# Performance work log

Measured on AMD Instinct MI355X. Metric: run time of the kernel, lower is better.

Reference implementation:

```python
import jax, jax.numpy as jnp
import numpy as np

H = 32          # num_attention_heads
KVH = 8         # num_key_value_heads
D = 2048        # hidden_size
HD = D // H     # attention_head_size = 64
REP = H // KVH  # queries per kv head = 4


def setup_inputs() -> dict:
    key = jax.random.key(0)
    ks = jax.random.split(key, 7)
    s = 0.02
    return {
        "hidden_states": jax.random.normal(ks[0], (2, 2048, D), dtype=jnp.float32),
        "Wq": jax.random.normal(ks[1], (D, D), dtype=jnp.float32) * s,
        "bq": jax.random.normal(ks[2], (D,), dtype=jnp.float32) * s,
        "Wk": jax.random.normal(ks[3], (D, KVH * HD), dtype=jnp.float32) * s,
        "bk": jax.random.normal(ks[4], (KVH * HD,), dtype=jnp.float32) * s,
        "Wv": jax.random.normal(ks[5], (D, KVH * HD), dtype=jnp.float32) * s,
        "bv": jax.random.normal(ks[6], (KVH * HD,), dtype=jnp.float32) * s,
    }


def _split_heads(x, n_heads):
    # [B, S, n_heads*HD] -> [B, n_heads, S, HD]
    b, s, _ = x.shape
    return x.reshape(b, s, n_heads, HD).transpose(0, 2, 1, 3)


def reference(hidden_states, Wq, bq, Wk, bk, Wv, bv):
    b, s, _ = hidden_states.shape
    q = _split_heads(hidden_states @ Wq + bq, H)          # [B,H,S,HD]
    k = _split_heads(hidden_states @ Wk + bk, KVH)        # [B,KVH,S,HD]
    v = _split_heads(hidden_states @ Wv + bv, KVH)
    # repeat KV heads to match query heads (q_idx // REP -> kv_idx)
    k = jnp.repeat(k, REP, axis=1)                         # [B,H,S,HD]
    v = jnp.repeat(v, REP, axis=1)
    scores = jnp.einsum("bhqd,bhkd->bhqk", q, k) / jnp.sqrt(jnp.float32(HD))
    probs = jax.nn.softmax(scores, axis=-1)
    ctx = jnp.einsum("bhqk,bhkd->bhqd", probs, v)          # [B,H,S,HD]
    ctx = ctx.transpose(0, 2, 1, 3).reshape(b, s, H * HD)
    return ctx
```

## Files before the change

kernel.cpp:

```cpp
#include <hip/hip_runtime.h>
#include <hip/hip_bf16.h>

#define NH 32
#define NKVH 8
#define DMODEL 2048
#define HDIM 64
#define NB 2
#define SEQ 2048
#define MROWS (NB*SEQ)
#define NQ 2048
#define NKV 512
#define NTOT 3072
#define NT (SEQ/64)

typedef __bf16 bf16x4 __attribute__((ext_vector_type(4)));
typedef __bf16 bf16x8 __attribute__((ext_vector_type(8)));
typedef float  f32x4  __attribute__((ext_vector_type(4)));
typedef float  f32x16 __attribute__((ext_vector_type(16)));
typedef unsigned u32x4 __attribute__((ext_vector_type(4)));

__device__ inline __bf16 f2bf(float f) {
    unsigned u = __builtin_bit_cast(unsigned, f);
    u += 0x7fff + ((u >> 16) & 1);
    unsigned short s = (unsigned short)(u >> 16);
    return __builtin_bit_cast(__bf16, s);
}

__device__ inline unsigned pack2bf(float a, float b) {
    unsigned ua = __builtin_bit_cast(unsigned, a);
    ua += 0x7fff + ((ua >> 16) & 1);
    unsigned ub = __builtin_bit_cast(unsigned, b);
    ub += 0x7fff + ((ub >> 16) & 1);
    return (ua >> 16) | (ub & 0xffff0000u);
}

__device__ inline void gload_lds16(const void* g, void* l) {
    __builtin_amdgcn_global_load_lds(
        (const __attribute__((address_space(1))) void*)g,
        (__attribute__((address_space(3))) void*)l, 16, 0, 0);
}

__global__ __launch_bounds__(256)
void cvt_hs(const float* __restrict__ Hs, __bf16* __restrict__ Ab)
{
    size_t idx = ((size_t)blockIdx.x * 256 + threadIdx.x) * 8;
    f32x4 a = *reinterpret_cast<const f32x4*>(Hs + idx);
    f32x4 b = *reinterpret_cast<const f32x4*>(Hs + idx + 4);
    u32x4 w;
    w[0] = pack2bf(a[0], a[1]); w[1] = pack2bf(a[2], a[3]);
    w[2] = pack2bf(b[0], b[1]); w[3] = pack2bf(b[2], b[3]);
    *reinterpret_cast<u32x4*>((char*)Ab + idx * 2) = w;
}

__global__ __launch_bounds__(256)
void transpose_w(const float* __restrict__ Wq,
                 const float* __restrict__ Wk,
                 const float* __restrict__ Wv,
                 __bf16* __restrict__ Wt)
{
    __shared__ __bf16 tile[64][72];
    int k0 = blockIdx.x * 64;
    int n0 = blockIdx.y * 64;
    const float* Wsrc; int ncols; int nbase;
    if (n0 < NQ)            { Wsrc = Wq; ncols = NQ;  nbase = n0; }
    else if (n0 < NQ + NKV) { Wsrc = Wk; ncols = NKV; nbase = n0 - NQ; }
    else                    { Wsrc = Wv; ncols = NKV; nbase = n0 - NQ - NKV; }
    int t = threadIdx.x;
    int kl = t >> 2;
    int nc = (t & 3) * 16;
    const float* src = Wsrc + (size_t)(k0 + kl) * ncols + nbase + nc;
    #pragma unroll
    for (int i = 0; i < 4; ++i) {
        f32x4 v = *reinterpret_cast<const f32x4*>(src + i * 4);
        #pragma unroll
        for (int e = 0; e < 4; ++e) tile[kl][nc + i * 4 + e] = f2bf(v[e]);
    }
    __syncthreads();
    int nl = t >> 2;
    int kc = (t & 3) * 16;
    bf16x8 o0, o1;
    #pragma unroll
    for (int i = 0; i < 8; ++i) o0[i] = tile[kc + i][nl];
    #pragma unroll
    for (int i = 0; i < 8; ++i) o1[i] = tile[kc + 8 + i][nl];
    __bf16* dst = Wt + (size_t)(n0 + nl) * DMODEL + k0 + kc;
    *reinterpret_cast<bf16x8*>(dst)     = o0;
    *reinterpret_cast<bf16x8*>(dst + 8) = o1;
}

#define BM 128
#define BN 128
#define BK 64

__global__ __launch_bounds__(256)
void qkv_gemm(const __bf16* __restrict__ Ab,
              const __bf16* __restrict__ Wt,
              const float* __restrict__ bq,
              const float* __restrict__ bk,
              const float* __restrict__ bv,
              __bf16* __restrict__ Qb,
              __bf16* __restrict__ Kb,
              __bf16* __restrict__ Vt)
{
    __shared__ char lds[32768];

    int bid = blockIdx.x;
    int wg = (bid & 7) * 96 + (bid >> 3);
    int n0 = (wg % 24) * BN;
    int m0 = (wg / 24) * BM;

    int t = threadIdx.x;
    int wave = t >> 6, lane = t & 63;
    int g = lane >> 4, lh = lane & 15;
    int wr = wave >> 1, wc = wave & 1;

    int srow = wave * 8 + (lane >> 3);
    int schunk = (lane & 7) ^ (lane >> 3);
    const char* Asrc = (const char*)Ab + (size_t)(m0 + srow) * 4096 + schunk * 16;
    const char* Bsrc = (const char*)Wt + (size_t)(n0 + srow) * 4096 + schunk * 16;
    int dstw = wave * 1024;

    f32x4 acc[4][4] = {};

    for (int k0 = 0; k0 < DMODEL * 2; k0 += BK * 2) {
        #pragma unroll
        for (int i = 0; i < 4; ++i)
            gload_lds16(Asrc + (size_t)i * 32 * 4096 + k0, lds + i * 4096 + dstw);
        #pragma unroll
        for (int i = 0; i < 4; ++i)
            gload_lds16(Bsrc + (size_t)i * 32 * 4096 + k0, lds + 16384 + i * 4096 + dstw);
        __syncthreads();
        #pragma unroll
        for (int kk = 0; kk < 2; ++kk) {
            bf16x8 af[4], bfr[4];
            #pragma unroll
            for (int mi = 0; mi < 4; ++mi) {
                int row = wr * 64 + mi * 16 + lh;
                int byte = row * 128 + (((kk * 4 + g) ^ (lh & 7)) << 4);
                af[mi] = *reinterpret_cast<const bf16x8*>(lds + byte);
            }
            #pragma unroll
            for (int ni = 0; ni < 4; ++ni) {
                int row = wc * 64 + ni * 16 + lh;
                int byte = row * 128 + (((kk * 4 + g) ^ (lh & 7)) << 4);
                bfr[ni] = *reinterpret_cast<const bf16x8*>(lds + 16384 + byte);
            }
            #pragma unroll
            for (int mi = 0; mi < 4; ++mi)
                #pragma unroll
                for (int ni = 0; ni < 4; ++ni)
                    acc[mi][ni] = __builtin_amdgcn_mfma_f32_16x16x32_bf16(af[mi], bfr[ni], acc[mi][ni], 0, 0, 0);
        }
        __syncthreads();
    }

    int mode = (n0 < NQ) ? 0 : (n0 < NQ + NKV ? 1 : 2);
    const float* bias = (mode == 0) ? bq : (mode == 1 ? bk : bv);
    int nsub = (mode == 0) ? 0 : (mode == 1 ? NQ : NQ + NKV);
    float scale = (mode == 0) ? 0.18033688011112042f : 1.0f;

    float biasv[4];
    #pragma unroll
    for (int ni = 0; ni < 4; ++ni)
        biasv[ni] = bias[n0 - nsub + wc * 64 + ni * 16 + lh];

    #pragma unroll
    for (int mi = 0; mi < 4; ++mi) {
        #pragma unroll
        for (int j = 0; j < 4; ++j) {
            int m = m0 + wr * 64 + mi * 16 + 4 * g + j;
            int bb = m >> 11, s = m & (SEQ - 1);
            #pragma unroll
            for (int ni = 0; ni < 4; ++ni) {
                int n = n0 + wc * 64 + ni * 16 + lh;
                __bf16 val = f2bf((acc[mi][ni][j] + biasv[ni]) * scale);
                if (mode == 0) {
                    int hh = n >> 6, d = n & 63;
                    Qb[(((size_t)bb * NH + hh) * SEQ + s) * HDIM + d] = val;
                } else if (mode == 1) {
                    int nk = n - NQ; int kv = nk >> 6, d = nk & 63;
                    Kb[(((size_t)bb * NKVH + kv) * SEQ + s) * HDIM + d] = val;
                } else {
                    int nv = n - NQ - NKV; int kv = nv >> 6, d = nv & 63;
                    Vt[(((size_t)bb * NKVH + kv) * HDIM + d) * SEQ + s] = val;
                }
            }
        }
    }
}

#define SUBSTEP(BUFB, SS) do { \
    bf16x8 kf0_ = *reinterpret_cast<const bf16x8*>(lds + (BUFB) + koff[(SS)*4 + 0]); \
    bf16x8 kf1_ = *reinterpret_cast<const bf16x8*>(lds + (BUFB) + koff[(SS)*4 + 1]); \
    bf16x8 kf2_ = *reinterpret_cast<const bf16x8*>(lds + (BUFB) + koff[(SS)*4 + 2]); \
    bf16x8 kf3_ = *reinterpret_cast<const bf16x8*>(lds + (BUFB) + koff[(SS)*4 + 3]); \
    f32x16 s_ = {}; \
    __builtin_amdgcn_s_setprio(1); \
    s_ = __builtin_amdgcn_mfma_f32_32x32x16_bf16(kf0_, qf[0], s_, 0, 0, 0); \
    s_ = __builtin_amdgcn_mfma_f32_32x32x16_bf16(kf1_, qf[1], s_, 0, 0, 0); \
    s_ = __builtin_amdgcn_mfma_f32_32x32x16_bf16(kf2_, qf[2], s_, 0, 0, 0); \
    s_ = __builtin_amdgcn_mfma_f32_32x32x16_bf16(kf3_, qf[3], s_, 0, 0, 0); \
    __builtin_amdgcn_s_setprio(0); \
    float m8_[8]; \
    _Pragma("unroll") \
    for (int r = 0; r < 8; ++r) m8_[r] = fmaxf(s_[r], s_[r + 8]); \
    float ml_ = fmaxf(fmaxf(fmaxf(fmaxf(fmaxf(fmaxf(fmaxf( \
        m8_[0], m8_[1]), m8_[2]), m8_[3]), m8_[4]), m8_[5]), m8_[6]), m8_[7]); \
    float mt_ = fmaxf(ml_, __shfl_xor(ml_, 32)); \
    if (!__all(mt_ <= m_run + 8.0f)) { \
        float mn_ = fmaxf(m_run, mt_); \
        float al_ = __builtin_amdgcn_exp2f(m_run - mn_); \
        m_run = mn_; l_run *= al_; accO0 *= al_; accO1 *= al_; \
    } \
    _Pragma("unroll") \
    for (int r = 0; r < 16; ++r) s_[r] = __builtin_amdgcn_exp2f(s_[r] - m_run); \
    float s8_[8]; \
    _Pragma("unroll") \
    for (int r = 0; r < 8; ++r) s8_[r] = s_[r] + s_[r + 8]; \
    float sum_ = ((s8_[0] + s8_[1]) + (s8_[2] + s8_[3])) + ((s8_[4] + s8_[5]) + (s8_[6] + s8_[7])); \
    l_run += sum_ + __shfl_xor(sum_, 32); \
    bf16x8 pa_, pb_; \
    _Pragma("unroll") \
    for (int e = 0; e < 8; ++e) { pa_[e] = (__bf16)s_[e]; pb_[e] = (__bf16)s_[8 + e]; } \
    bf16x8 va0_ = *reinterpret_cast<const bf16x8*>(lds + (BUFB) + 8192 + koff[2 * (SS)]); \
    bf16x8 vb0_ = *reinterpret_cast<const bf16x8*>(lds + (BUFB) + 8192 + koff[2 * (SS) + 1]); \
    bf16x8 va1_ = *reinterpret_cast<const bf16x8*>(lds + (BUFB) + 8192 + koff[4 + 2 * (SS)]); \
    bf16x8 vb1_ = *reinterpret_cast<const bf16x8*>(lds + (BUFB) + 8192 + koff[4 + 2 * (SS) + 1]); \
    __builtin_amdgcn_s_setprio(1); \
    accO0 = __builtin_amdgcn_mfma_f32_32x32x16_bf16(va0_, pa_, accO0, 0, 0, 0); \
    accO0 = __builtin_amdgcn_mfma_f32_32x32x16_bf16(vb0_, pb_, accO0, 0, 0, 0); \
    accO1 = __builtin_amdgcn_mfma_f32_32x32x16_bf16(va1_, pa_, accO1, 0, 0, 0); \
    accO1 = __builtin_amdgcn_mfma_f32_32x32x16_bf16(vb1_, pb_, accO1, 0, 0, 0); \
    __builtin_amdgcn_s_setprio(0); \
} while (0)

#define TILE(BUFB, NBUFB, KT, MORE) do { \
    if (MORE) { \
        const char* gk_ = Kp + (size_t)((KT) + 1) * 8192; \
        gload_lds16(gk_ + kgoff0, lds + (NBUFB) + kdst0); \
        gload_lds16(gk_ + kgoff1, lds + (NBUFB) + kdst1); \
        const char* gv_ = Vp + vgoff + (size_t)((KT) + 1) * 128; \
        v0r = *reinterpret_cast<const bf16x8*>(gv_); \
        v1r = *reinterpret_cast<const bf16x8*>(gv_ + 16); \
    } \
    SUBSTEP(BUFB, 0); \
    SUBSTEP(BUFB, 1); \
    if (MORE) { \
        bf16x8 cA_ = __builtin_shufflevector(v0r, v1r, 0, 1, 2, 3, 8, 9, 10, 11); \
        bf16x8 cB_ = __builtin_shufflevector(v0r, v1r, 4, 5, 6, 7, 12, 13, 14, 15); \
        *reinterpret_cast<bf16x8*>(lds + (NBUFB) + vwoffA)        = cA_; \
        *reinterpret_cast<bf16x8*>(lds + (NBUFB) + (vwoffA ^ 16)) = cB_; \
    } \
    __syncthreads(); \
} while (0)

__global__ __launch_bounds__(256, 4)
void attn(const __bf16* __restrict__ Qb,
          const __bf16* __restrict__ Kb,
          const __bf16* __restrict__ Vt,
          float* __restrict__ out)
{
    __shared__ char lds[32768];

    int qt = blockIdx.x;
    int bh = blockIdx.y;
    int b = bh >> 5, h = bh & 31;
    int kvh = h >> 2;
    int tid = threadIdx.x, wave = tid >> 6, lane = tid & 63;
    int ql = lane & 31, hi = lane >> 5;
    int q0 = qt * 128 + wave * 32;

    const __bf16* Qp = Qb + (size_t)(b * NH + h) * SEQ * HDIM;
    const char*   Kp = (const char*)(Kb + (size_t)(b * NKVH + kvh) * SEQ * HDIM);
    const char*   Vp = (const char*)(Vt + (size_t)(b * NKVH + kvh) * HDIM * SEQ);

    bf16x8 qf[4];
    #pragma unroll
    for (int f = 0; f < 4; ++f)
        qf[f] = *reinterpret_cast<const bf16x8*>(Qp + (size_t)(q0 + ql) * HDIM + f * 16 + hi * 8);

    int Mq = (ql & 7) << 4;
    int kgoff0 = wave * 1024 + ((lane >> 3) << 7) + (((lane & 7) ^ (lane >> 3)) << 4);
    int kgoff1 = kgoff0 + 4096;
    int kdst0 = wave * 1024;
    int kdst1 = kdst0 + 4096;
    int vd = wave * 16 + (lane >> 2);
    int vc = lane & 3;
    size_t vgoff = (size_t)vd * (SEQ * 2) + vc * 32;
    int Mv = (vd & 7) << 4;
    int vwoffA = 8192 + vd * 128 + ((vc * 32) ^ Mv);
    int koff[8];
    #pragma unroll
    for (int kb = 0; kb < 2; ++kb)
        #pragma unroll
        for (int f = 0; f < 4; ++f)
            koff[kb * 4 + f] = (kb * 32 + ql) * 128 + ((f * 32 + hi * 16) ^ Mq);

    f32x16 accO0 = {}, accO1 = {};
    float m_run = -1e30f, l_run = 0.0f;

    bf16x8 v0r, v1r;

    gload_lds16(Kp + kgoff0, lds + kdst0);
    gload_lds16(Kp + kgoff1, lds + kdst1);
    {
        const char* gv = Vp + vgoff;
        v0r = *reinterpret_cast<const bf16x8*>(gv);
        v1r = *reinterpret_cast<const bf16x8*>(gv + 16);
        bf16x8 cA = __builtin_shufflevector(v0r, v1r, 0, 1, 2, 3, 8, 9, 10, 11);
        bf16x8 cB = __builtin_shufflevector(v0r, v1r, 4, 5, 6, 7, 12, 13, 14, 15);
        *reinterpret_cast<bf16x8*>(lds + vwoffA)        = cA;
        *reinterpret_cast<bf16x8*>(lds + (vwoffA ^ 16)) = cB;
    }
    __syncthreads();

    #pragma unroll 1
    for (int kt2 = 0; kt2 < 15; ++kt2) {
        TILE(0,     16384, 2 * kt2,     true);
        TILE(16384, 0,     2 * kt2 + 1, true);
    }
    TILE(0,     16384, 30, true);
    TILE(16384, 0,     31, false);

    float inv = 1.0f / l_run;
    float* op = out + ((size_t)b * SEQ + q0 + ql) * DMODEL + h * HDIM;
    #pragma unroll
    for (int G = 0; G < 4; ++G) {
        f32x4 o0 = { accO0[4 * G + 0] * inv, accO0[4 * G + 1] * inv,
                     accO0[4 * G + 2] * inv, accO0[4 * G + 3] * inv };
        f32x4 o1 = { accO1[4 * G + 0] * inv, accO1[4 * G + 1] * inv,
                     accO1[4 * G + 2] * inv, accO1[4 * G + 3] * inv };
        *reinterpret_cast<f32x4*>(op + 8 * G + 4 * hi)      = o0;
        *reinterpret_cast<f32x4*>(op + 32 + 8 * G + 4 * hi) = o1;
    }
}

extern "C" void kernel_launch(void* const* d_in, const int* in_sizes, int n_in,
                              void* d_out, int out_size, void* d_ws, size_t ws_size,
                              hipStream_t stream)
{
    const float* hs = (const float*)d_in[0];
    const float* Wq = (const float*)d_in[1];
    const float* bq = (const float*)d_in[2];
    const float* Wk = (const float*)d_in[3];
    const float* bk = (const float*)d_in[4];
    const float* Wv = (const float*)d_in[5];
    const float* bv = (const float*)d_in[6];
    float* out = (float*)d_out;

    char* ws = (char*)d_ws;
    __bf16* Wt = (__bf16*)(ws);
    __bf16* Ab = (__bf16*)(ws + 12582912);
    __bf16* Qb = (__bf16*)(ws + 12582912 + 16777216);
    __bf16* Kb = (__bf16*)(ws + 12582912 + 2*16777216);
    __bf16* Vt = (__bf16*)(ws + 12582912 + 2*16777216 + 4194304);

    hipLaunchKernelGGL(cvt_hs,      dim3(4096),   dim3(256), 0, stream, hs, Ab);
    hipLaunchKernelGGL(transpose_w, dim3(32, 48), dim3(256), 0, stream, Wq, Wk, Wv, Wt);
    hipLaunchKernelGGL(qkv_gemm,    dim3(768),    dim3(256), 0, stream, Ab, Wt, bq, bk, bv, Qb, Kb, Vt);
    hipLaunchKernelGGL(attn,        dim3(16, 64), dim3(256), 0, stream, Qb, Kb, Vt, out);
}
```

Baseline: 189.4 us.

## Compute softmax row sums via MFMA with ones, use max3 and permlane32 swap

Replaces the VALU reduction of softmax probabilities with extra MFMA ops that multiply the bf16 P fragments by a ones vector, accumulating the row sum in a matrix accumulator. Row max now uses v_max3 inline asm and a permlane32_swap cross-half exchange instead of a shuffle. The running max subtraction is folded into a precomputed negated offset. This adds two MFMAs per substep and a 16-register accumulator, so launch bounds drop occupancy from 4 to 3 blocks per CU, and the sum now comes from bf16-rounded probabilities.

```diff
diff --git a/kernel.cpp b/kernel.cpp
--- a/kernel.cpp
+++ b/kernel.cpp
@@ -15,8 +15,10 @@
 
 typedef __bf16 bf16x4 __attribute__((ext_vector_type(4)));
 typedef __bf16 bf16x8 __attribute__((ext_vector_type(8)));
+typedef float  f32x2  __attribute__((ext_vector_type(2)));
 typedef float  f32x4  __attribute__((ext_vector_type(4)));
 typedef float  f32x16 __attribute__((ext_vector_type(16)));
+typedef unsigned u32x2 __attribute__((ext_vector_type(2)));
 typedef unsigned u32x4 __attribute__((ext_vector_type(4)));
 
 __device__ inline __bf16 f2bf(float f) {
@@ -38,6 +40,22 @@
     __builtin_amdgcn_global_load_lds(
         (const __attribute__((address_space(1))) void*)g,
         (__attribute__((address_space(3))) void*)l, 16, 0, 0);
+}
+
+__device__ inline float max3f(float a, float b, float c) {
+    float r;
+    asm("v_max3_f32 %0, %1, %2, %3" : "=v"(r) : "v"(a), "v"(b), "v"(c));
+    return r;
+}
+
+__device__ inline float cross_max32(float x) {
+#if __has_builtin(__builtin_amdgcn_permlane32_swap)
+    unsigned xu = __builtin_bit_cast(unsigned, x);
+    u32x2 r = __builtin_amdgcn_permlane32_swap(xu, xu, false, false);
+    return fmaxf(__builtin_bit_cast(float, r[0]), __builtin_bit_cast(float, r[1]));
+#else
+    return fmaxf(x, __shfl_xor(x, 32));
+#endif
 }
 
 __global__ __launch_bounds__(256)
@@ -201,24 +219,18 @@
     s_ = __builtin_amdgcn_mfma_f32_32x32x16_bf16(kf2_, qf[2], s_, 0, 0, 0); \
     s_ = __builtin_amdgcn_mfma_f32_32x32x16_bf16(kf3_, qf[3], s_, 0, 0, 0); \
     __builtin_amdgcn_s_setprio(0); \
-    float m8_[8]; \
-    _Pragma("unroll") \
-    for (int r = 0; r < 8; ++r) m8_[r] = fmaxf(s_[r], s_[r + 8]); \
-    float ml_ = fmaxf(fmaxf(fmaxf(fmaxf(fmaxf(fmaxf(fmaxf( \
-        m8_[0], m8_[1]), m8_[2]), m8_[3]), m8_[4]), m8_[5]), m8_[6]), m8_[7]); \
-    float mt_ = fmaxf(ml_, __shfl_xor(ml_, 32)); \
+    float n0_ = max3f(max3f(s_[0], s_[1], s_[2]),  max3f(s_[3], s_[4], s_[5]), \
+                      max3f(s_[6], s_[7], s_[8])); \
+    float n1_ = max3f(max3f(s_[9], s_[10], s_[11]), max3f(s_[12], s_[13], s_[14]), s_[15]); \
+    float mt_ = cross_max32(fmaxf(n0_, n1_)); \
     if (!__all(mt_ <= m_run + 8.0f)) { \
         float mn_ = fmaxf(m_run, mt_); \
         float al_ = __builtin_amdgcn_exp2f(m_run - mn_); \
-        m_run = mn_; l_run *= al_; accO0 *= al_; accO1 *= al_; \
+        m_run = mn_; msub = -mn_; \
+        accO0 *= al_; accO1 *= al_; lsum *= al_; \
     } \
     _Pragma("unroll") \
-    for (int r = 0; r < 16; ++r) s_[r] = __builtin_amdgcn_exp2f(s_[r] - m_run); \
-    float s8_[8]; \
-    _Pragma("unroll") \
-    for (int r = 0; r < 8; ++r) s8_[r] = s_[r] + s_[r + 8]; \
-    float sum_ = ((s8_[0] + s8_[1]) + (s8_[2] + s8_[3])) + ((s8_[4] + s8_[5]) + (s8_[6] + s8_[7])); \
-    l_run += sum_ + __shfl_xor(sum_, 32); \
+    for (int r = 0; r < 16; ++r) s_[r] = __builtin_amdgcn_exp2f(s_[r] + msub); \
     bf16x8 pa_, pb_; \
     _Pragma("unroll") \
     for (int e = 0; e < 8; ++e) { pa_[e] = (__bf16)s_[e]; pb_[e] = (__bf16)s_[8 + e]; } \
@@ -228,7 +240,9 @@
     bf16x8 vb1_ = *reinterpret_cast<const bf16x8*>(lds + (BUFB) + 8192 + koff[4 + 2 * (SS) + 1]); \
     __builtin_amdgcn_s_setprio(1); \
     accO0 = __builtin_amdgcn_mfma_f32_32x32x16_bf16(va0_, pa_, accO0, 0, 0, 0); \
+    lsum  = __builtin_amdgcn_mfma_f32_32x32x16_bf16(ones, pa_, lsum,  0, 0, 0); \
     accO0 = __builtin_amdgcn_mfma_f32_32x32x16_bf16(vb0_, pb_, accO0, 0, 0, 0); \
+    lsum  = __builtin_amdgcn_mfma_f32_32x32x16_bf16(ones, pb_, lsum,  0, 0, 0); \
     accO1 = __builtin_amdgcn_mfma_f32_32x32x16_bf16(va1_, pa_, accO1, 0, 0, 0); \
     accO1 = __builtin_amdgcn_mfma_f32_32x32x16_bf16(vb1_, pb_, accO1, 0, 0, 0); \
     __builtin_amdgcn_s_setprio(0); \
@@ -254,7 +268,7 @@
     __syncthreads(); \
 } while (0)
 
-__global__ __launch_bounds__(256, 4)
+__global__ __launch_bounds__(256, 3)
 void attn(const __bf16* __restrict__ Qb,
           const __bf16* __restrict__ Kb,
           const __bf16* __restrict__ Vt,
@@ -278,6 +292,9 @@
     #pragma unroll
     for (int f = 0; f < 4; ++f)
         qf[f] = *reinterpret_cast<const bf16x8*>(Qp + (size_t)(q0 + ql) * HDIM + f * 16 + hi * 8);
+
+    u32x4 ou = { 0x3F803F80u, 0x3F803F80u, 0x3F803F80u, 0x3F803F80u };
+    bf16x8 ones = __builtin_bit_cast(bf16x8, ou);
 
     int Mq = (ql & 7) << 4;
     int kgoff0 = wave * 1024 + ((lane >> 3) << 7) + (((lane & 7) ^ (lane >> 3)) << 4);
@@ -296,8 +313,8 @@
         for (int f = 0; f < 4; ++f)
             koff[kb * 4 + f] = (kb * 32 + ql) * 128 + ((f * 32 + hi * 16) ^ Mq);
 
-    f32x16 accO0 = {}, accO1 = {};
-    float m_run = -1e30f, l_run = 0.0f;
+    f32x16 accO0 = {}, accO1 = {}, lsum = {};
+    float m_run = -1e30f, msub = 0.0f;
 
     bf16x8 v0r, v1r;
 
@@ -322,7 +339,7 @@
     TILE(0,     16384, 30, true);
     TILE(16384, 0,     31, false);
 
-    float inv = 1.0f / l_run;
+    float inv = 1.0f / lsum[0];
     float* op = out + ((size_t)b * SEQ + q0 + ql) * DMODEL + h * HDIM;
     #pragma unroll
     for (int G = 0; G < 4; ++G) {
```

New measurement: 189.5 us. No clear change (+0.1%).
